# Kernel optimization log

Measured on AMD Instinct MI355X. Metric: run time of the kernel, lower is better.

Reference implementation:

```python
import jax, jax.numpy as jnp
import numpy as np

UP = 2  # scale factor

def make_kernel(vals, factor):
    k = jnp.asarray(vals, dtype=jnp.float32)
    k = k[None, :] * k[:, None]          # 1D -> separable 2D
    k = k / k.sum()
    return k * (factor ** 2)             # gain for upsampling

def setup_inputs() -> dict:
    key = jax.random.key(0)
    x = jax.random.normal(key, (8, 128, 128, 128), dtype=jnp.float32)
    kernel = make_kernel([1.0, 3.0, 3.0, 1.0], UP)  # (4,4)
    return {"inp_tensor": x, "kernel": kernel}

def reference(inp_tensor, kernel):
    # upfirdn2d(x, k, up=2, down=1, pad=(pad0, pad1)) fused via dilated conv:
    # lhs_dilation performs the zero-insertion upsample without materializing
    # the big zero tensor; extra (UP-1) right/bottom pad matches StyleGAN2's
    # trailing zeros after zero-insertion.
    kh, kw = kernel.shape
    p = kh - UP
    pad0 = (p + 1) // 2 + UP - 1
    pad1 = p // 2
    n, c, h, w = inp_tensor.shape
    x = inp_tensor.reshape(n * c, 1, h, w)
    # torch impl does F.conv2d with flipped kernel == true convolution with k;
    # lax conv is correlation, so flip to match (k is symmetric here anyway).
    wk = jnp.flip(kernel, (0, 1))[None, None]  # (1,1,kh,kw)
    out = jax.lax.conv_general_dilated(
        x, wk,
        window_strides=(1, 1),
        padding=((pad0, pad1 + UP - 1), (pad0, pad1 + UP - 1)),
        lhs_dilation=(UP, UP),
        dimension_numbers=("NCHW", "OIHW", "NCHW"),
    )
    return out.reshape(n, c, h * UP, w * UP)
```

## Files before the change

kernel.cpp:

```cpp
#include <hip/hip_runtime.h>

#define NC   1024
#define H    128
#define W    128
#define OH   256
#define OW   256


__device__ __forceinline__ void accum(float L, const float4& v, float R,
                                      const float4& kr, float o[8]) {
    float e1 = kr.y, e3 = kr.w;
    float c0 = kr.x, c2 = kr.z;
    o[0] += e1 * v.x + e3 * L;
    o[1] += c0 * v.y + c2 * v.x;
    o[2] += e1 * v.y + e3 * v.x;
    o[3] += c0 * v.z + c2 * v.y;
    o[4] += e1 * v.z + e3 * v.y;
    o[5] += c0 * v.w + c2 * v.z;
    o[6] += e1 * v.w + e3 * v.z;
    o[7] += c0 * R   + c2 * v.w;
}

__global__ __launch_bounds__(256) void upscale_kernel(
    const float* __restrict__ x,
    const float* __restrict__ Kp,
    float* __restrict__ out)
{
    int gid = blockIdx.x * blockDim.x + threadIdx.x;
    int jg = gid & 31;
    int iy = (gid >> 5) & (H - 1);
    int nc = gid >> 12;

    const float4* row = (const float4*)(x + (size_t)nc * (H * W));
    const float4 z = make_float4(0.f, 0.f, 0.f, 0.f);

    float4 vm = (iy > 0)     ? row[(size_t)(iy - 1) * (W / 4) + jg] : z;
    float4 v0 =                row[(size_t)iy       * (W / 4) + jg];
    float4 vp = (iy < H - 1) ? row[(size_t)(iy + 1) * (W / 4) + jg] : z;

    float Lm = __shfl_up(vm.w, 1, 32);
    float L0 = __shfl_up(v0.w, 1, 32);
    float Lp = __shfl_up(vp.w, 1, 32);
    float Rm = __shfl_down(vm.x, 1, 32);
    float R0 = __shfl_down(v0.x, 1, 32);
    float Rp = __shfl_down(vp.x, 1, 32);
    if (jg == 0)     { Lm = 0.f; L0 = 0.f; Lp = 0.f; }
    if (jg == W/4-1) { Rm = 0.f; R0 = 0.f; Rp = 0.f; }

    const float4* K4 = (const float4*)Kp;
    float4 k0 = K4[0], k1 = K4[1], k2 = K4[2], k3 = K4[3];

    float oe[8] = {0.f, 0.f, 0.f, 0.f, 0.f, 0.f, 0.f, 0.f};
    accum(L0, v0, R0, k1, oe);
    accum(Lm, vm, Rm, k3, oe);
    float oo[8] = {0.f, 0.f, 0.f, 0.f, 0.f, 0.f, 0.f, 0.f};
    accum(L0, v0, R0, k2, oo);
    accum(Lp, vp, Rp, k0, oo);

    float* ob = out + (size_t)nc * (OH * OW) + (size_t)(2 * iy) * OW + 8 * jg;
    ((float4*)ob)[0] = make_float4(oe[0], oe[1], oe[2], oe[3]);
    ((float4*)ob)[1] = make_float4(oe[4], oe[5], oe[6], oe[7]);
    float* ob2 = ob + OW;
    ((float4*)ob2)[0] = make_float4(oo[0], oo[1], oo[2], oo[3]);
    ((float4*)ob2)[1] = make_float4(oo[4], oo[5], oo[6], oo[7]);
}

extern "C" void kernel_launch(void* const* d_in, const int* in_sizes, int n_in,
                              void* d_out, int out_size, void* d_ws, size_t ws_size,
                              hipStream_t stream) {
    const float* x   = (const float*)d_in[0];
    const float* K   = (const float*)d_in[1];
    float*       out = (float*)d_out;

    const int total_threads = NC * H * (W / 4);
    dim3 block(256);
    dim3 grid(total_threads / 256);
    upscale_kernel<<<grid, block, 0, stream>>>(x, K, out);
}
```

Baseline: 335.0 us.

## Process 8-row bands per wave with sliding row window to reuse loads

```diff
diff --git a/kernel.cpp b/kernel.cpp
--- a/kernel.cpp
+++ b/kernel.cpp
@@ -1,24 +1,29 @@
 #include <hip/hip_runtime.h>
 
-#define NC   1024
-#define H    128
-#define W    128
-#define OH   256
-#define OW   256
+#define NC    1024
+#define H     128
+#define W     128
+#define OH    256
+#define OW    256
+#define ROWS  8
+#define BANDS (H / ROWS)
 
 
-__device__ __forceinline__ void accum(float L, const float4& v, float R,
-                                      const float4& kr, float o[8]) {
-    float e1 = kr.y, e3 = kr.w;
-    float c0 = kr.x, c2 = kr.z;
-    o[0] += e1 * v.x + e3 * L;
-    o[1] += c0 * v.y + c2 * v.x;
-    o[2] += e1 * v.y + e3 * v.x;
-    o[3] += c0 * v.z + c2 * v.y;
-    o[4] += e1 * v.z + e3 * v.y;
-    o[5] += c0 * v.w + c2 * v.z;
-    o[6] += e1 * v.w + e3 * v.z;
-    o[7] += c0 * R   + c2 * v.w;
+struct Row { float L, a, b, R; };
+
+__device__ __forceinline__ Row load_row(const float* __restrict__ base,
+                                        int r, int lane) {
+    float2 v = make_float2(0.f, 0.f);
+    if ((unsigned)r < (unsigned)H)
+        v = ((const float2*)(base + (size_t)r * W))[lane];
+    Row o;
+    o.a = v.x;
+    o.b = v.y;
+    o.L = __shfl_up(v.y, 1, 64);
+    o.R = __shfl_down(v.x, 1, 64);
+    if (lane == 0)  o.L = 0.f;
+    if (lane == 63) o.R = 0.f;
+    return o;
 }
 
 __global__ __launch_bounds__(256) void upscale_kernel(
@@ -26,43 +31,44 @@
     const float* __restrict__ Kp,
     float* __restrict__ out)
 {
-    int gid = blockIdx.x * blockDim.x + threadIdx.x;
-    int jg = gid & 31;
-    int iy = (gid >> 5) & (H - 1);
-    int nc = gid >> 12;
+    const int lane = threadIdx.x & 63;
+    const int wave = blockIdx.x * (256 >> 6) + (threadIdx.x >> 6);
+    const int band = wave & (BANDS - 1);
+    const int nc   = wave >> 4;
+    const int r0   = band * ROWS;
 
-    const float4* row = (const float4*)(x + (size_t)nc * (H * W));
-    const float4 z = make_float4(0.f, 0.f, 0.f, 0.f);
+    const float* __restrict__ base = x   + (size_t)nc * (H * W);
+    float*       __restrict__ ob   = out + (size_t)nc * (OH * OW);
 
-    float4 vm = (iy > 0)     ? row[(size_t)(iy - 1) * (W / 4) + jg] : z;
-    float4 v0 =                row[(size_t)iy       * (W / 4) + jg];
-    float4 vp = (iy < H - 1) ? row[(size_t)(iy + 1) * (W / 4) + jg] : z;
+    const float k00 = Kp[0],  k01 = Kp[1],  k02 = Kp[2],  k03 = Kp[3];
+    const float k10 = Kp[4],  k11 = Kp[5],  k12 = Kp[6],  k13 = Kp[7];
+    const float k20 = Kp[8],  k21 = Kp[9],  k22 = Kp[10], k23 = Kp[11];
+    const float k30 = Kp[12], k31 = Kp[13], k32 = Kp[14], k33 = Kp[15];
 
-    float Lm = __shfl_up(vm.w, 1, 32);
-    float L0 = __shfl_up(v0.w, 1, 32);
-    float Lp = __shfl_up(vp.w, 1, 32);
-    float Rm = __shfl_down(vm.x, 1, 32);
-    float R0 = __shfl_down(v0.x, 1, 32);
-    float Rp = __shfl_down(vp.x, 1, 32);
-    if (jg == 0)     { Lm = 0.f; L0 = 0.f; Lp = 0.f; }
-    if (jg == W/4-1) { Rm = 0.f; R0 = 0.f; Rp = 0.f; }
+    Row m = load_row(base, r0 - 1, lane);
+    Row c = load_row(base, r0,     lane);
 
-    const float4* K4 = (const float4*)Kp;
-    float4 k0 = K4[0], k1 = K4[1], k2 = K4[2], k3 = K4[3];
+    #pragma unroll
+    for (int i = 0; i < ROWS; ++i) {
+        const int r = r0 + i;
+        Row p = load_row(base, r + 1, lane);
 
-    float oe[8] = {0.f, 0.f, 0.f, 0.f, 0.f, 0.f, 0.f, 0.f};
-    accum(L0, v0, R0, k1, oe);
-    accum(Lm, vm, Rm, k3, oe);
-    float oo[8] = {0.f, 0.f, 0.f, 0.f, 0.f, 0.f, 0.f, 0.f};
-    accum(L0, v0, R0, k2, oo);
-    accum(Lp, vp, Rp, k0, oo);
+        float4 oe, oo;
+        oe.x = k11 * c.a + k13 * c.L + k31 * m.a + k33 * m.L;
+        oe.y = k10 * c.b + k12 * c.a + k30 * m.b + k32 * m.a;
+        oe.z = k11 * c.b + k13 * c.a + k31 * m.b + k33 * m.a;
+        oe.w = k10 * c.R + k12 * c.b + k30 * m.R + k32 * m.b;
+        oo.x = k21 * c.a + k23 * c.L + k01 * p.a + k03 * p.L;
+        oo.y = k20 * c.b + k22 * c.a + k00 * p.b + k02 * p.a;
+        oo.z = k21 * c.b + k23 * c.a + k01 * p.b + k03 * p.a;
+        oo.w = k20 * c.R + k22 * c.b + k00 * p.R + k02 * p.b;
 
-    float* ob = out + (size_t)nc * (OH * OW) + (size_t)(2 * iy) * OW + 8 * jg;
-    ((float4*)ob)[0] = make_float4(oe[0], oe[1], oe[2], oe[3]);
-    ((float4*)ob)[1] = make_float4(oe[4], oe[5], oe[6], oe[7]);
-    float* ob2 = ob + OW;
-    ((float4*)ob2)[0] = make_float4(oo[0], oo[1], oo[2], oo[3]);
-    ((float4*)ob2)[1] = make_float4(oo[4], oo[5], oo[6], oo[7]);
+        ((float4*)(ob + (size_t)(2 * r)     * OW))[lane] = oe;
+        ((float4*)(ob + (size_t)(2 * r + 1) * OW))[lane] = oo;
+
+        m = c;
+        c = p;
+    }
 }
 
 extern "C" void kernel_launch(void* const* d_in, const int* in_sizes, int n_in,
@@ -72,8 +78,8 @@
     const float* K   = (const float*)d_in[1];
     float*       out = (float*)d_out;
 
-    const int total_threads = NC * H * (W / 4);
+    const int total_waves = NC * BANDS;
     dim3 block(256);
-    dim3 grid(total_threads / 256);
+    dim3 grid(total_waves / 4);
     upscale_kernel<<<grid, block, 0, stream>>>(x, K, out);
 }
```

Result: faster. 310.7 us (-7.2%).
